# Optimization experiments

Measured on AMD Instinct MI355X. Metric: run time of the kernel, lower is better.

The kernel has to match this reference:

```python
import jax, jax.numpy as jnp
import numpy as np

T, D, I, E, G, LG, K = 2048, 1024, 512, 32, 8, 4, 6
SI = 2 * I  # shared expert inter dim = n_shared_experts * inter_dim
ROUTE_SCALE = 1.0


def setup_inputs() -> dict:
    key = jax.random.key(0)
    ks = jax.random.split(key, 16)
    s = 0.02
    f = jnp.float32
    return {
        "x": jax.random.normal(ks[0], (T, D), f),
        "router_w": jax.random.normal(ks[1], (E, D), f) * s,
        "router_b": jax.random.normal(ks[2], (E,), f) * s,
        "W1": jax.random.normal(ks[3], (E, D, I), f) * s,
        "b1": jax.random.normal(ks[4], (E, I), f) * s,
        "W2": jax.random.normal(ks[5], (E, D, I), f) * s,
        "b2": jax.random.normal(ks[6], (E, I), f) * s,
        "W3": jax.random.normal(ks[7], (E, I, D), f) * s,
        "b3": jax.random.normal(ks[8], (E, D), f) * s,
        "sw1": jax.random.normal(ks[9], (D, SI), f) * s,
        "sb1": jax.random.normal(ks[10], (SI,), f) * s,
        "sw2": jax.random.normal(ks[11], (D, SI), f) * s,
        "sb2": jax.random.normal(ks[12], (SI,), f) * s,
        "sw3": jax.random.normal(ks[13], (SI, D), f) * s,
        "sb3": jax.random.normal(ks[14], (D,), f) * s,
    }


def _route(x, router_w, router_b):
    # Router: softmax scores (fp32), group-limited top-k.
    logits = x @ router_w.T + router_b                      # [T, E]
    scores = jax.nn.softmax(logits.astype(jnp.float32), axis=-1)
    original = scores
    sg = scores.reshape(x.shape[0], G, E // G)              # [T, G, E/G]
    # no router bias -> group score = sum of top-2 expert scores per group
    group_scores = jnp.sum(jax.lax.top_k(sg, 2)[0], axis=-1)  # [T, G]
    _, gidx = jax.lax.top_k(group_scores, LG)               # [T, LG]
    keep = jnp.zeros((x.shape[0], G), bool).at[jnp.arange(x.shape[0])[:, None], gidx].set(True)
    masked = jnp.where(keep[:, :, None], sg, -jnp.inf).reshape(x.shape[0], E)
    _, idx = jax.lax.top_k(masked, K)                       # [T, K]
    vals = jnp.take_along_axis(original, idx, axis=1) * ROUTE_SCALE
    return vals.astype(x.dtype), idx


def reference(x, router_w, router_b, W1, b1, W2, b2, W3, b3, sw1, sb1, sw2, sb2, sw3, sb3):
    vals, idx = _route(x, router_w, router_b)
    # dense gate matrix [T, E]; top-k indices per row are distinct
    gates = jnp.zeros((x.shape[0], E), x.dtype).at[jnp.arange(x.shape[0])[:, None], idx].set(vals)
    # routed experts: Expert(x) = W3 @ silu(w1(x) * w2(x))
    h1 = jnp.einsum('td,edi->tei', x, W1) + b1              # [T, E, I]
    h2 = jnp.einsum('td,edi->tei', x, W2) + b2
    h = jax.nn.silu(h1 * h2)
    y = jnp.einsum('tei,eid->td', h * gates[:, :, None], W3) + gates @ b3
    # shared expert
    z = jax.nn.silu((x @ sw1 + sb1) * (x @ sw2 + sb2)) @ sw3 + sb3
    return y + z
```

## Files before the change

kernel.cpp:

```cpp
#include <hip/hip_runtime.h>
#include <hip/hip_bf16.h>
#include <math.h>

#define T_CONST 2048
#define D_CONST 1024
#define I_CONST 512
#define SI_CONST 1024
#define E_CONST 32
#define G_CONST 8
#define LG_CONST 4
#define KSEL 6

#define BM 128
#define BN 64
#define BK 32

typedef __attribute__((ext_vector_type(8))) short short8;
typedef __attribute__((ext_vector_type(4))) float floatx4;

__device__ inline unsigned pack_bf16(float a, float b) {
  __hip_bfloat162 h = __float22bfloat162_rn(float2{a, b});
  return *reinterpret_cast<unsigned*>(&h);
}

__global__ __launch_bounds__(256) void router_kernel(
    const float* __restrict__ x, const float* __restrict__ rw,
    const float* __restrict__ rb, int* __restrict__ counts,
    int* __restrict__ slots, float* __restrict__ gatel) {
  int t = blockIdx.x;
  __shared__ float sx[D_CONST];
  __shared__ float slog[E_CONST];
  int tid = threadIdx.x;
  for (int i = tid; i < D_CONST; i += 256) sx[i] = x[(size_t)t * D_CONST + i];
  __syncthreads();
  int e = tid >> 3, l8 = tid & 7;
  float s = 0.f;
  const float* rwp = rw + (size_t)e * D_CONST;
  for (int d = l8; d < D_CONST; d += 8) s += sx[d] * rwp[d];
  s += __shfl_xor(s, 4, 8);
  s += __shfl_xor(s, 2, 8);
  s += __shfl_xor(s, 1, 8);
  if (l8 == 0) slog[e] = s + rb[e];
  __syncthreads();
  if (tid == 0) {
    float sc[E_CONST];
    float mx = -1e30f;
    for (int i = 0; i < E_CONST; ++i) mx = fmaxf(mx, slog[i]);
    float sum = 0.f;
    for (int i = 0; i < E_CONST; ++i) { sc[i] = expf(slog[i] - mx); sum += sc[i]; }
    float inv = 1.f / sum;
    for (int i = 0; i < E_CONST; ++i) sc[i] *= inv;
    float gs[G_CONST];
    for (int g = 0; g < G_CONST; ++g) {
      float m1 = -1e30f, m2 = -1e30f;
      for (int j = 0; j < 4; ++j) {
        float v = sc[g * 4 + j];
        if (v > m1) { m2 = m1; m1 = v; }
        else if (v > m2) { m2 = v; }
      }
      gs[g] = m1 + m2;
    }
    bool keep[G_CONST];
    for (int g = 0; g < G_CONST; ++g) keep[g] = false;
    for (int r = 0; r < LG_CONST; ++r) {
      int bi = -1; float bv = -1e30f;
      for (int g = 0; g < G_CONST; ++g)
        if (!keep[g] && gs[g] > bv) { bv = gs[g]; bi = g; }
      keep[bi] = true;
    }
    bool taken[E_CONST];
    for (int i = 0; i < E_CONST; ++i) taken[i] = false;
    for (int r = 0; r < KSEL; ++r) {
      int bi = -1; float bv = -1e30f;
      for (int i = 0; i < E_CONST; ++i)
        if (keep[i >> 2] && !taken[i] && sc[i] > bv) { bv = sc[i]; bi = i; }
      taken[bi] = true;
      int pos = atomicAdd(&counts[bi], 1);
      slots[bi * T_CONST + pos] = t * KSEL + r;
      gatel[bi * T_CONST + pos] = sc[bi];
    }
  }
}

template <bool GATHER>
__global__ __launch_bounds__(256, 2) void up_proj_mfma(
    const float* __restrict__ X, const float* __restrict__ W1g,
    const float* __restrict__ W2g, const float* __restrict__ bias1,
    const float* __restrict__ bias2, const int* __restrict__ counts,
    const int* __restrict__ slots, __hip_bfloat16* __restrict__ Hout, int N) {
  const int e = GATHER ? blockIdx.z : 0;
  const int cnt = GATHER ? counts[e] : T_CONST;
  const int m0 = blockIdx.y * BM;
  if (m0 >= cnt) return;
  const int n0 = blockIdx.x * BN;

  __shared__ short As[4 * BM * 8];
  __shared__ short Bs1[4 * BN * 8];
  __shared__ short Bs2[4 * BN * 8];
  __shared__ int srow[BM];
  __shared__ int sdst[BM];

  const int tid = threadIdx.x;
  for (int i = tid; i < BM; i += 256) {
    int r = m0 + i;
    bool valid = r < cnt;
    if (GATHER) {
      int sl = valid ? slots[e * T_CONST + r] : 0;
      srow[i] = valid ? sl / KSEL : 0;
      sdst[i] = valid ? sl : -1;
    } else {
      srow[i] = valid ? r : 0;
      sdst[i] = valid ? r : -1;
    }
  }
  __syncthreads();

  const float* Wp1 = W1g + (size_t)e * D_CONST * N;
  const float* Wp2 = W2g + (size_t)e * D_CONST * N;

  const int lane = tid & 63;
  const int wave = tid >> 6;
  const int wm = wave & 1, wn = wave >> 1;
  const int l15 = lane & 15, quad = lane >> 4;

  floatx4 acc1[4][2] = {};
  floatx4 acc2[4][2] = {};

  const int akq = tid & 7;
  const float* aptr[4];
#pragma unroll
  for (int it = 0; it < 4; ++it) {
    int m = (tid >> 3) + 32 * it;
    aptr[it] = X + (size_t)srow[m] * D_CONST + akq * 4;
  }
  const int bkp = tid >> 4, bnq = tid & 15;
  const int bc = bkp >> 2, bj = (bkp & 3) * 2;

  for (int kk = 0; kk < D_CONST; kk += BK) {
#pragma unroll
    for (int it = 0; it < 4; ++it) {
      int m = (tid >> 3) + 32 * it;
      float4 f = *(const float4*)(aptr[it] + kk);
      uint2 u;
      u.x = pack_bf16(f.x, f.y);
      u.y = pack_bf16(f.z, f.w);
      int c = akq >> 1, h = akq & 1;
      *(uint2*)&As[(c * BM + m) * 8 + h * 4] = u;
    }
    {
      int k = kk + bkp * 2;
      int n = n0 + bnq * 4;
      const float* p1 = Wp1 + (size_t)k * N + n;
      const float* p2 = Wp2 + (size_t)k * N + n;
      float4 r0 = *(const float4*)p1;
      float4 r1 = *(const float4*)(p1 + N);
      float4 q0 = *(const float4*)p2;
      float4 q1 = *(const float4*)(p2 + N);
      int nb = bnq * 4;
      *(unsigned*)&Bs1[(bc * BN + nb + 0) * 8 + bj] = pack_bf16(r0.x, r1.x);
      *(unsigned*)&Bs1[(bc * BN + nb + 1) * 8 + bj] = pack_bf16(r0.y, r1.y);
      *(unsigned*)&Bs1[(bc * BN + nb + 2) * 8 + bj] = pack_bf16(r0.z, r1.z);
      *(unsigned*)&Bs1[(bc * BN + nb + 3) * 8 + bj] = pack_bf16(r0.w, r1.w);
      *(unsigned*)&Bs2[(bc * BN + nb + 0) * 8 + bj] = pack_bf16(q0.x, q1.x);
      *(unsigned*)&Bs2[(bc * BN + nb + 1) * 8 + bj] = pack_bf16(q0.y, q1.y);
      *(unsigned*)&Bs2[(bc * BN + nb + 2) * 8 + bj] = pack_bf16(q0.z, q1.z);
      *(unsigned*)&Bs2[(bc * BN + nb + 3) * 8 + bj] = pack_bf16(q0.w, q1.w);
    }
    __syncthreads();

    short8 a[4];
#pragma unroll
    for (int mi = 0; mi < 4; ++mi)
      a[mi] = *(const short8*)&As[(quad * BM + wm * 64 + mi * 16 + l15) * 8];
#pragma unroll
    for (int ni = 0; ni < 2; ++ni) {
      short8 b1 = *(const short8*)&Bs1[(quad * BN + wn * 32 + ni * 16 + l15) * 8];
      short8 b2 = *(const short8*)&Bs2[(quad * BN + wn * 32 + ni * 16 + l15) * 8];
#pragma unroll
      for (int mi = 0; mi < 4; ++mi) {
        acc1[mi][ni] = __builtin_amdgcn_mfma_f32_16x16x32_bf16(a[mi], b1, acc1[mi][ni], 0, 0, 0);
        acc2[mi][ni] = __builtin_amdgcn_mfma_f32_16x16x32_bf16(a[mi], b2, acc2[mi][ni], 0, 0, 0);
      }
    }
    __syncthreads();
  }

  const float* bb1 = bias1 + (size_t)e * N + n0;
  const float* bb2 = bias2 + (size_t)e * N + n0;
#pragma unroll
  for (int mi = 0; mi < 4; ++mi) {
#pragma unroll
    for (int ni = 0; ni < 2; ++ni) {
      int n = wn * 32 + ni * 16 + l15;
      float c1 = bb1[n], c2 = bb2[n];
#pragma unroll
      for (int reg = 0; reg < 4; ++reg) {
        int row = wm * 64 + mi * 16 + quad * 4 + reg;
        int dst = sdst[row];
        if (dst < 0) continue;
        float h1 = acc1[mi][ni][reg] + c1;
        float h2 = acc2[mi][ni][reg] + c2;
        float p = h1 * h2;
        float s = p / (1.f + expf(-p));
        Hout[(size_t)dst * N + n0 + n] = __float2bfloat16(s);
      }
    }
  }
}

template <bool ROUTED>
__global__ __launch_bounds__(256, 2) void down_proj_mfma(
    const __hip_bfloat16* __restrict__ Hin, const float* __restrict__ Wd,
    const float* __restrict__ bd, const int* __restrict__ counts,
    const int* __restrict__ slots, const float* __restrict__ gatel,
    float* __restrict__ Out, int Kdim) {
  const int e = ROUTED ? blockIdx.z : 0;
  const int cnt = ROUTED ? counts[e] : T_CONST;
  const int m0 = blockIdx.y * BM;
  if (m0 >= cnt) return;
  const int n0 = blockIdx.x * BN;

  __shared__ short As[4 * BM * 8];
  __shared__ short Bs[4 * BN * 8];
  __shared__ int ssrc[BM];
  __shared__ int stok[BM];
  __shared__ float sg[BM];

  const int tid = threadIdx.x;
  for (int i = tid; i < BM; i += 256) {
    int r = m0 + i;
    bool valid = r < cnt;
    if (ROUTED) {
      int sl = valid ? slots[e * T_CONST + r] : 0;
      ssrc[i] = sl;
      stok[i] = valid ? (sl / KSEL) : -1;
      sg[i] = valid ? gatel[e * T_CONST + r] : 0.f;
    } else {
      ssrc[i] = valid ? r : 0;
      stok[i] = valid ? r : -1;
      sg[i] = 1.f;
    }
  }
  __syncthreads();

  const float* Wp = Wd + (size_t)e * Kdim * D_CONST;

  const int lane = tid & 63;
  const int wave = tid >> 6;
  const int wm = wave & 1, wn = wave >> 1;
  const int l15 = lane & 15, quad = lane >> 4;

  floatx4 acc[4][2] = {};

  const int ako = tid & 3;
  const __hip_bfloat16* aptr[2];
#pragma unroll
  for (int it = 0; it < 2; ++it) {
    int m = (tid >> 2) + 64 * it;
    aptr[it] = Hin + (size_t)ssrc[m] * Kdim + ako * 8;
  }
  const int bkp = tid >> 4, bnq = tid & 15;
  const int bc = bkp >> 2, bj = (bkp & 3) * 2;

  for (int kk = 0; kk < Kdim; kk += BK) {
#pragma unroll
    for (int it = 0; it < 2; ++it) {
      int m = (tid >> 2) + 64 * it;
      uint4 v = *(const uint4*)(aptr[it] + kk);
      *(uint4*)&As[(ako * BM + m) * 8] = v;
    }
    {
      int k = kk + bkp * 2;
      int n = n0 + bnq * 4;
      const float* p = Wp + (size_t)k * D_CONST + n;
      float4 r0 = *(const float4*)p;
      float4 r1 = *(const float4*)(p + D_CONST);
      int nb = bnq * 4;
      *(unsigned*)&Bs[(bc * BN + nb + 0) * 8 + bj] = pack_bf16(r0.x, r1.x);
      *(unsigned*)&Bs[(bc * BN + nb + 1) * 8 + bj] = pack_bf16(r0.y, r1.y);
      *(unsigned*)&Bs[(bc * BN + nb + 2) * 8 + bj] = pack_bf16(r0.z, r1.z);
      *(unsigned*)&Bs[(bc * BN + nb + 3) * 8 + bj] = pack_bf16(r0.w, r1.w);
    }
    __syncthreads();

    short8 a[4];
#pragma unroll
    for (int mi = 0; mi < 4; ++mi)
      a[mi] = *(const short8*)&As[(quad * BM + wm * 64 + mi * 16 + l15) * 8];
#pragma unroll
    for (int ni = 0; ni < 2; ++ni) {
      short8 b = *(const short8*)&Bs[(quad * BN + wn * 32 + ni * 16 + l15) * 8];
#pragma unroll
      for (int mi = 0; mi < 4; ++mi)
        acc[mi][ni] = __builtin_amdgcn_mfma_f32_16x16x32_bf16(a[mi], b, acc[mi][ni], 0, 0, 0);
    }
    __syncthreads();
  }

#pragma unroll
  for (int mi = 0; mi < 4; ++mi) {
#pragma unroll
    for (int ni = 0; ni < 2; ++ni) {
      int n = n0 + wn * 32 + ni * 16 + l15;
      float bias = ROUTED ? bd[(size_t)e * D_CONST + n] : bd[n];
#pragma unroll
      for (int reg = 0; reg < 4; ++reg) {
        int row = wm * 64 + mi * 16 + quad * 4 + reg;
        int tok = stok[row];
        if (tok < 0) continue;
        if (ROUTED) {
          float v = sg[row] * (acc[mi][ni][reg] + bias);
          atomicAdd(&Out[(size_t)tok * D_CONST + n], v);
        } else {
          Out[(size_t)tok * D_CONST + n] = acc[mi][ni][reg] + bias;
        }
      }
    }
  }
}

extern "C" void kernel_launch(void* const* d_in, const int* in_sizes, int n_in,
                              void* d_out, int out_size, void* d_ws, size_t ws_size,
                              hipStream_t stream) {
  const float* x   = (const float*)d_in[0];
  const float* rw  = (const float*)d_in[1];
  const float* rb  = (const float*)d_in[2];
  const float* W1  = (const float*)d_in[3];
  const float* b1  = (const float*)d_in[4];
  const float* W2  = (const float*)d_in[5];
  const float* b2  = (const float*)d_in[6];
  const float* W3  = (const float*)d_in[7];
  const float* b3  = (const float*)d_in[8];
  const float* sw1 = (const float*)d_in[9];
  const float* sb1 = (const float*)d_in[10];
  const float* sw2 = (const float*)d_in[11];
  const float* sb2 = (const float*)d_in[12];
  const float* sw3 = (const float*)d_in[13];
  const float* sb3 = (const float*)d_in[14];
  float* out = (float*)d_out;

  char* w = (char*)d_ws;
  int* counts = (int*)w;
  int* slots = (int*)(w + 256);
  float* gatel = (float*)(w + 256 + E_CONST * T_CONST * 4);
  __hip_bfloat16* Hbuf = (__hip_bfloat16*)(w + 256 + 2 * E_CONST * T_CONST * 4);
  __hip_bfloat16* Hs = (__hip_bfloat16*)(w + 256 + 2 * E_CONST * T_CONST * 4 +
                                         (size_t)T_CONST * KSEL * I_CONST * 2);

  hipMemsetAsync(counts, 0, E_CONST * sizeof(int), stream);
  router_kernel<<<T_CONST, 256, 0, stream>>>(x, rw, rb, counts, slots, gatel);
  up_proj_mfma<true><<<dim3(I_CONST / BN, T_CONST / BM, E_CONST), 256, 0, stream>>>(
      x, W1, W2, b1, b2, counts, slots, Hbuf, I_CONST);
  up_proj_mfma<false><<<dim3(SI_CONST / BN, T_CONST / BM, 1), 256, 0, stream>>>(
      x, sw1, sw2, sb1, sb2, nullptr, nullptr, Hs, SI_CONST);
  down_proj_mfma<false><<<dim3(D_CONST / BN, T_CONST / BM, 1), 256, 0, stream>>>(
      Hs, sw3, sb3, nullptr, nullptr, nullptr, out, SI_CONST);
  down_proj_mfma<true><<<dim3(D_CONST / BN, T_CONST / BM, E_CONST), 256, 0, stream>>>(
      Hbuf, W3, b3, counts, slots, gatel, out, I_CONST);
}
```

Before: 545.4 us.

## Pre-transpose weights to bf16, use direct global-to-LDS loads, parallelize router

```diff
diff --git a/kernel.cpp b/kernel.cpp
--- a/kernel.cpp
+++ b/kernel.cpp
@@ -13,7 +13,7 @@
 
 #define BM 128
 #define BN 64
-#define BK 32
+#define BK 64
 
 typedef __attribute__((ext_vector_type(8))) short short8;
 typedef __attribute__((ext_vector_type(4))) float floatx4;
@@ -23,165 +23,238 @@
   return *reinterpret_cast<unsigned*>(&h);
 }
 
-__global__ __launch_bounds__(256) void router_kernel(
-    const float* __restrict__ x, const float* __restrict__ rw,
+__device__ inline void gload16(const void* g, void* l) {
+  __builtin_amdgcn_global_load_lds(
+      (const __attribute__((address_space(1))) unsigned int*)g,
+      (__attribute__((address_space(3))) unsigned int*)l, 16, 0, 0);
+}
+
+__global__ __launch_bounds__(256) void cvt_x(const float* __restrict__ in,
+                                             __hip_bfloat16* __restrict__ out) {
+  size_t i = ((size_t)blockIdx.x * 256 + threadIdx.x) * 4;
+  float4 v = *(const float4*)&in[i];
+  uint2 u{pack_bf16(v.x, v.y), pack_bf16(v.z, v.w)};
+  *(uint2*)&out[i] = u;
+}
+
+__global__ __launch_bounds__(256) void cvt_rwt(const float* __restrict__ rw,
+                                               float* __restrict__ rwt) {
+  int i = blockIdx.x * 256 + threadIdx.x;
+  int d = i >> 5, e = i & 31;
+  rwt[d * 32 + e] = rw[e * D_CONST + d];
+}
+
+__global__ __launch_bounds__(256) void transpose_all(
+    const float* __restrict__ W1, const float* __restrict__ W2,
+    const float* __restrict__ W3, const float* __restrict__ sw1,
+    const float* __restrict__ sw2, const float* __restrict__ sw3,
+    __hip_bfloat16* __restrict__ W1t, __hip_bfloat16* __restrict__ W2t,
+    __hip_bfloat16* __restrict__ W3t, __hip_bfloat16* __restrict__ sw1t,
+    __hip_bfloat16* __restrict__ sw2t, __hip_bfloat16* __restrict__ sw3t) {
+  __shared__ float tile[64][65];
+  int b = blockIdx.x;
+  const float* in;
+  __hip_bfloat16* out;
+  int K, N, k0, n0;
+  if (b < 8192) {
+    int local = b & 4095;
+    int mat = local >> 7, rem = local & 127;
+    K = 1024; N = 512;
+    in = ((b < 4096) ? W1 : W2) + (size_t)mat * (1024 * 512);
+    out = ((b < 4096) ? W1t : W2t) + (size_t)mat * (1024 * 512);
+    n0 = (rem & 7) * 64; k0 = (rem >> 3) * 64;
+  } else if (b < 12288) {
+    int local = b - 8192;
+    int mat = local >> 7, rem = local & 127;
+    K = 512; N = 1024;
+    in = W3 + (size_t)mat * (512 * 1024);
+    out = W3t + (size_t)mat * (512 * 1024);
+    n0 = (rem & 15) * 64; k0 = (rem >> 4) * 64;
+  } else {
+    int local = b - 12288;
+    int which = local >> 8, rem = local & 255;
+    K = 1024; N = 1024;
+    in = which == 0 ? sw1 : which == 1 ? sw2 : sw3;
+    out = which == 0 ? sw1t : which == 1 ? sw2t : sw3t;
+    n0 = (rem & 15) * 64; k0 = (rem >> 4) * 64;
+  }
+  int tid = threadIdx.x;
+  int tr = tid >> 4, tc4 = (tid & 15) * 4;
+#pragma unroll
+  for (int i = 0; i < 4; ++i) {
+    float4 v = *(const float4*)&in[(size_t)(k0 + tr + 16 * i) * N + n0 + tc4];
+    tile[tr + 16 * i][tc4 + 0] = v.x;
+    tile[tr + 16 * i][tc4 + 1] = v.y;
+    tile[tr + 16 * i][tc4 + 2] = v.z;
+    tile[tr + 16 * i][tc4 + 3] = v.w;
+  }
+  __syncthreads();
+#pragma unroll
+  for (int i = 0; i < 4; ++i) {
+    int n = tr + 16 * i;
+    unsigned lo = pack_bf16(tile[tc4 + 0][n], tile[tc4 + 1][n]);
+    unsigned hi = pack_bf16(tile[tc4 + 2][n], tile[tc4 + 3][n]);
+    uint2 u{lo, hi};
+    *(uint2*)&out[(size_t)(n0 + n) * K + k0 + tc4] = u;
+  }
+}
+
+__global__ __launch_bounds__(256) void router2(
+    const float* __restrict__ x, const float* __restrict__ rwt,
     const float* __restrict__ rb, int* __restrict__ counts,
     int* __restrict__ slots, float* __restrict__ gatel) {
-  int t = blockIdx.x;
-  __shared__ float sx[D_CONST];
-  __shared__ float slog[E_CONST];
-  int tid = threadIdx.x;
-  for (int i = tid; i < D_CONST; i += 256) sx[i] = x[(size_t)t * D_CONST + i];
-  __syncthreads();
-  int e = tid >> 3, l8 = tid & 7;
+  const int lane = threadIdx.x & 63;
+  const int wv = threadIdx.x >> 6;
+  const int t = blockIdx.x * 4 + wv;
+  const int e = lane & 31, h = lane >> 5;
+  const float* xp = x + (size_t)t * D_CONST;
   float s = 0.f;
-  const float* rwp = rw + (size_t)e * D_CONST;
-  for (int d = l8; d < D_CONST; d += 8) s += sx[d] * rwp[d];
-  s += __shfl_xor(s, 4, 8);
-  s += __shfl_xor(s, 2, 8);
-  s += __shfl_xor(s, 1, 8);
-  if (l8 == 0) slog[e] = s + rb[e];
-  __syncthreads();
-  if (tid == 0) {
-    float sc[E_CONST];
-    float mx = -1e30f;
-    for (int i = 0; i < E_CONST; ++i) mx = fmaxf(mx, slog[i]);
-    float sum = 0.f;
-    for (int i = 0; i < E_CONST; ++i) { sc[i] = expf(slog[i] - mx); sum += sc[i]; }
-    float inv = 1.f / sum;
-    for (int i = 0; i < E_CONST; ++i) sc[i] *= inv;
-    float gs[G_CONST];
-    for (int g = 0; g < G_CONST; ++g) {
-      float m1 = -1e30f, m2 = -1e30f;
-      for (int j = 0; j < 4; ++j) {
-        float v = sc[g * 4 + j];
-        if (v > m1) { m2 = m1; m1 = v; }
-        else if (v > m2) { m2 = v; }
-      }
-      gs[g] = m1 + m2;
-    }
-    bool keep[G_CONST];
-    for (int g = 0; g < G_CONST; ++g) keep[g] = false;
-    for (int r = 0; r < LG_CONST; ++r) {
-      int bi = -1; float bv = -1e30f;
-      for (int g = 0; g < G_CONST; ++g)
-        if (!keep[g] && gs[g] > bv) { bv = gs[g]; bi = g; }
-      keep[bi] = true;
-    }
-    bool taken[E_CONST];
-    for (int i = 0; i < E_CONST; ++i) taken[i] = false;
-    for (int r = 0; r < KSEL; ++r) {
-      int bi = -1; float bv = -1e30f;
-      for (int i = 0; i < E_CONST; ++i)
-        if (keep[i >> 2] && !taken[i] && sc[i] > bv) { bv = sc[i]; bi = i; }
-      taken[bi] = true;
-      int pos = atomicAdd(&counts[bi], 1);
-      slots[bi * T_CONST + pos] = t * KSEL + r;
-      gatel[bi * T_CONST + pos] = sc[bi];
-    }
+#pragma unroll 8
+  for (int d = h; d < D_CONST; d += 2) s = fmaf(xp[d], rwt[d * 32 + e], s);
+  s += __shfl_xor(s, 32);
+  s += rb[e];
+  float mx = s;
+#pragma unroll
+  for (int m = 16; m >= 1; m >>= 1) mx = fmaxf(mx, __shfl_xor(mx, m));
+  float p = expf(s - mx);
+  float sum = p;
+#pragma unroll
+  for (int m = 16; m >= 1; m >>= 1) sum += __shfl_xor(sum, m);
+  float sc = p / sum;
+  float a = sc, bb = __shfl_xor(a, 1);
+  float hi = fmaxf(a, bb), lo = fminf(a, bb);
+  float oh = __shfl_xor(hi, 2), ol = __shfl_xor(lo, 2);
+  float gs = fmaxf(fmaxf(hi + oh, hi + lo), oh + ol);
+  const int g = e >> 2;
+  unsigned keep = 0;
+  float gv = gs;
+#pragma unroll
+  for (int r = 0; r < LG_CONST; ++r) {
+    float v = gv;
+    int gi = g;
+#pragma unroll
+    for (int m = 16; m >= 1; m >>= 1) {
+      float ov = __shfl_xor(v, m);
+      int og = __shfl_xor(gi, m);
+      if (ov > v || (ov == v && og < gi)) { v = ov; gi = og; }
+    }
+    keep |= 1u << gi;
+    if (g == gi) gv = -1e30f;
+  }
+  float cand = ((keep >> g) & 1u) ? sc : -1e30f;
+  int sel_e = -1;
+  float sel_v = 0.f;
+#pragma unroll
+  for (int r = 0; r < KSEL; ++r) {
+    float v = cand;
+    int ei = e;
+#pragma unroll
+    for (int m = 16; m >= 1; m >>= 1) {
+      float ov = __shfl_xor(v, m);
+      int oe = __shfl_xor(ei, m);
+      if (ov > v || (ov == v && oe < ei)) { v = ov; ei = oe; }
+    }
+    if (lane == r) { sel_e = ei; sel_v = v; }
+    if (e == ei) cand = -1e30f;
+  }
+  if (lane < KSEL) {
+    int pos = atomicAdd(&counts[sel_e], 1);
+    slots[sel_e * T_CONST + pos] = t * KSEL + lane;
+    gatel[sel_e * T_CONST + pos] = sel_v;
   }
 }
 
 template <bool GATHER>
-__global__ __launch_bounds__(256, 2) void up_proj_mfma(
-    const float* __restrict__ X, const float* __restrict__ W1g,
-    const float* __restrict__ W2g, const float* __restrict__ bias1,
+__global__ __launch_bounds__(256, 2) void up_mfma2(
+    const __hip_bfloat16* __restrict__ Abf, const __hip_bfloat16* __restrict__ B1t,
+    const __hip_bfloat16* __restrict__ B2t, const float* __restrict__ bias1,
     const float* __restrict__ bias2, const int* __restrict__ counts,
-    const int* __restrict__ slots, __hip_bfloat16* __restrict__ Hout, int N) {
+    const int* __restrict__ slots, __hip_bfloat16* __restrict__ Hout,
+    int N, int Kd) {
   const int e = GATHER ? blockIdx.z : 0;
   const int cnt = GATHER ? counts[e] : T_CONST;
   const int m0 = blockIdx.y * BM;
   if (m0 >= cnt) return;
   const int n0 = blockIdx.x * BN;
 
-  __shared__ short As[4 * BM * 8];
-  __shared__ short Bs1[4 * BN * 8];
-  __shared__ short Bs2[4 * BN * 8];
+  __shared__ short As[8 * BM * 8];
+  __shared__ short Bs1[8 * BN * 8];
+  __shared__ short Bs2[8 * BN * 8];
   __shared__ int srow[BM];
   __shared__ int sdst[BM];
 
   const int tid = threadIdx.x;
-  for (int i = tid; i < BM; i += 256) {
-    int r = m0 + i;
+  const int lane = tid & 63, wv = tid >> 6;
+  if (tid < BM) {
+    int r = m0 + tid;
     bool valid = r < cnt;
     if (GATHER) {
       int sl = valid ? slots[e * T_CONST + r] : 0;
-      srow[i] = valid ? sl / KSEL : 0;
-      sdst[i] = valid ? sl : -1;
+      srow[tid] = valid ? sl / KSEL : 0;
+      sdst[tid] = valid ? sl : -1;
     } else {
-      srow[i] = valid ? r : 0;
-      sdst[i] = valid ? r : -1;
+      srow[tid] = valid ? r : 0;
+      sdst[tid] = valid ? r : -1;
     }
   }
   __syncthreads();
 
-  const float* Wp1 = W1g + (size_t)e * D_CONST * N;
-  const float* Wp2 = W2g + (size_t)e * D_CONST * N;
-
-  const int lane = tid & 63;
-  const int wave = tid >> 6;
-  const int wm = wave & 1, wn = wave >> 1;
+  const char* agp[4];
+  short* alds[4];
+  const char* bgp[4];
+  short* blds[4];
+  {
+    int row0 = srow[lane], row1 = srow[64 + lane];
+#pragma unroll
+    for (int i = 0; i < 4; ++i) {
+      int kc = 2 * wv + (i >> 1);
+      int mh = i & 1;
+      agp[i] = (const char*)(Abf + (size_t)(mh ? row1 : row0) * Kd + kc * 8);
+      alds[i] = (short*)As + (kc * BM + mh * 64 + lane) * 8;
+    }
+    const __hip_bfloat16* Bsel = (wv < 2 ? B1t : B2t) + (size_t)e * N * Kd;
+    short* Lsel = (wv < 2) ? (short*)Bs1 : (short*)Bs2;
+    int wl = wv & 1;
+#pragma unroll
+    for (int i = 0; i < 4; ++i) {
+      int kc = wl * 4 + i;
+      bgp[i] = (const char*)(Bsel + (size_t)(n0 + lane) * Kd + kc * 8);
+      blds[i] = Lsel + (kc * BN + lane) * 8;
+    }
+  }
+
   const int l15 = lane & 15, quad = lane >> 4;
-
+  const int wm = wv & 1, wn = wv >> 1;
   floatx4 acc1[4][2] = {};
   floatx4 acc2[4][2] = {};
-
-  const int akq = tid & 7;
-  const float* aptr[4];
-#pragma unroll
-  for (int it = 0; it < 4; ++it) {
-    int m = (tid >> 3) + 32 * it;
-    aptr[it] = X + (size_t)srow[m] * D_CONST + akq * 4;
-  }
-  const int bkp = tid >> 4, bnq = tid & 15;
-  const int bc = bkp >> 2, bj = (bkp & 3) * 2;
-
-  for (int kk = 0; kk < D_CONST; kk += BK) {
-#pragma unroll
-    for (int it = 0; it < 4; ++it) {
-      int m = (tid >> 3) + 32 * it;
-      float4 f = *(const float4*)(aptr[it] + kk);
-      uint2 u;
-      u.x = pack_bf16(f.x, f.y);
-      u.y = pack_bf16(f.z, f.w);
-      int c = akq >> 1, h = akq & 1;
-      *(uint2*)&As[(c * BM + m) * 8 + h * 4] = u;
-    }
-    {
-      int k = kk + bkp * 2;
-      int n = n0 + bnq * 4;
-      const float* p1 = Wp1 + (size_t)k * N + n;
-      const float* p2 = Wp2 + (size_t)k * N + n;
-      float4 r0 = *(const float4*)p1;
-      float4 r1 = *(const float4*)(p1 + N);
-      float4 q0 = *(const float4*)p2;
-      float4 q1 = *(const float4*)(p2 + N);
-      int nb = bnq * 4;
-      *(unsigned*)&Bs1[(bc * BN + nb + 0) * 8 + bj] = pack_bf16(r0.x, r1.x);
-      *(unsigned*)&Bs1[(bc * BN + nb + 1) * 8 + bj] = pack_bf16(r0.y, r1.y);
-      *(unsigned*)&Bs1[(bc * BN + nb + 2) * 8 + bj] = pack_bf16(r0.z, r1.z);
-      *(unsigned*)&Bs1[(bc * BN + nb + 3) * 8 + bj] = pack_bf16(r0.w, r1.w);
-      *(unsigned*)&Bs2[(bc * BN + nb + 0) * 8 + bj] = pack_bf16(q0.x, q1.x);
-      *(unsigned*)&Bs2[(bc * BN + nb + 1) * 8 + bj] = pack_bf16(q0.y, q1.y);
-      *(unsigned*)&Bs2[(bc * BN + nb + 2) * 8 + bj] = pack_bf16(q0.z, q1.z);
-      *(unsigned*)&Bs2[(bc * BN + nb + 3) * 8 + bj] = pack_bf16(q0.w, q1.w);
-    }
+  const int kiter = Kd / BK;
+
+  for (int it = 0; it < kiter; ++it) {
+#pragma unroll
+    for (int i = 0; i < 4; ++i) gload16(agp[i], alds[i]);
+#pragma unroll
+    for (int i = 0; i < 4; ++i) gload16(bgp[i], blds[i]);
+#pragma unroll
+    for (int i = 0; i < 4; ++i) { agp[i] += BK * 2; bgp[i] += BK * 2; }
     __syncthreads();
-
-    short8 a[4];
-#pragma unroll
-    for (int mi = 0; mi < 4; ++mi)
-      a[mi] = *(const short8*)&As[(quad * BM + wm * 64 + mi * 16 + l15) * 8];
-#pragma unroll
-    for (int ni = 0; ni < 2; ++ni) {
-      short8 b1 = *(const short8*)&Bs1[(quad * BN + wn * 32 + ni * 16 + l15) * 8];
-      short8 b2 = *(const short8*)&Bs2[(quad * BN + wn * 32 + ni * 16 + l15) * 8];
-#pragma unroll
-      for (int mi = 0; mi < 4; ++mi) {
-        acc1[mi][ni] = __builtin_amdgcn_mfma_f32_16x16x32_bf16(a[mi], b1, acc1[mi][ni], 0, 0, 0);
-        acc2[mi][ni] = __builtin_amdgcn_mfma_f32_16x16x32_bf16(a[mi], b2, acc2[mi][ni], 0, 0, 0);
+    short8 a[2][4];
+#pragma unroll
+    for (int s = 0; s < 2; ++s)
+#pragma unroll
+      for (int mi = 0; mi < 4; ++mi)
+        a[s][mi] = *(const short8*)&As[((s * 4 + quad) * BM + wm * 64 + mi * 16 + l15) * 8];
+#pragma unroll
+    for (int s = 0; s < 2; ++s)
+#pragma unroll
+      for (int ni = 0; ni < 2; ++ni) {
+        short8 b1 = *(const short8*)&Bs1[((s * 4 + quad) * BN + wn * 32 + ni * 16 + l15) * 8];
+        short8 b2 = *(const short8*)&Bs2[((s * 4 + quad) * BN + wn * 32 + ni * 16 + l15) * 8];
+#pragma unroll
+        for (int mi = 0; mi < 4; ++mi) {
+          acc1[mi][ni] = __builtin_amdgcn_mfma_f32_16x16x32_bf16(a[s][mi], b1, acc1[mi][ni], 0, 0, 0);
+          acc2[mi][ni] = __builtin_amdgcn_mfma_f32_16x16x32_bf16(a[s][mi], b2, acc2[mi][ni], 0, 0, 0);
+        }
       }
-    }
     __syncthreads();
   }
 
@@ -201,99 +274,101 @@
         float h1 = acc1[mi][ni][reg] + c1;
         float h2 = acc2[mi][ni][reg] + c2;
         float p = h1 * h2;
-        float s = p / (1.f + expf(-p));
-        Hout[(size_t)dst * N + n0 + n] = __float2bfloat16(s);
+        float sv = p / (1.f + expf(-p));
+        Hout[(size_t)dst * N + n0 + n] = __float2bfloat16(sv);
       }
     }
   }
 }
 
 template <bool ROUTED>
-__global__ __launch_bounds__(256, 2) void down_proj_mfma(
-    const __hip_bfloat16* __restrict__ Hin, const float* __restrict__ Wd,
+__global__ __launch_bounds__(256, 2) void down_mfma2(
+    const __hip_bfloat16* __restrict__ Hin, const __hip_bfloat16* __restrict__ Bt,
     const float* __restrict__ bd, const int* __restrict__ counts,
     const int* __restrict__ slots, const float* __restrict__ gatel,
-    float* __restrict__ Out, int Kdim) {
+    float* __restrict__ Out, int Kd) {
   const int e = ROUTED ? blockIdx.z : 0;
   const int cnt = ROUTED ? counts[e] : T_CONST;
   const int m0 = blockIdx.y * BM;
   if (m0 >= cnt) return;
   const int n0 = blockIdx.x * BN;
 
-  __shared__ short As[4 * BM * 8];
-  __shared__ short Bs[4 * BN * 8];
+  __shared__ short As[8 * BM * 8];
+  __shared__ short Bs[8 * BN * 8];
   __shared__ int ssrc[BM];
   __shared__ int stok[BM];
   __shared__ float sg[BM];
 
   const int tid = threadIdx.x;
-  for (int i = tid; i < BM; i += 256) {
-    int r = m0 + i;
+  const int lane = tid & 63, wv = tid >> 6;
+  if (tid < BM) {
+    int r = m0 + tid;
     bool valid = r < cnt;
     if (ROUTED) {
       int sl = valid ? slots[e * T_CONST + r] : 0;
-      ssrc[i] = sl;
-      stok[i] = valid ? (sl / KSEL) : -1;
-      sg[i] = valid ? gatel[e * T_CONST + r] : 0.f;
+      ssrc[tid] = sl;
+      stok[tid] = valid ? (sl / KSEL) : -1;
+      sg[tid] = valid ? gatel[e * T_CONST + r] : 0.f;
     } else {
-      ssrc[i] = valid ? r : 0;
-      stok[i] = valid ? r : -1;
-      sg[i] = 1.f;
+      ssrc[tid] = valid ? r : 0;
+      stok[tid] = valid ? r : -1;
+      sg[tid] = 1.f;
     }
   }
   __syncthreads();
 
-  const float* Wp = Wd + (size_t)e * Kdim * D_CONST;
-
-  const int lane = tid & 63;
-  const int wave = tid >> 6;
-  const int wm = wave & 1, wn = wave >> 1;
+  const char* agp[4];
+  short* alds[4];
+  const char* bgp[2];
+  short* blds[2];
+  {
+    int row0 = ssrc[lane], row1 = ssrc[64 + lane];
+#pragma unroll
+    for (int i = 0; i < 4; ++i) {
+      int kc = 2 * wv + (i >> 1);
+      int mh = i & 1;
+      agp[i] = (const char*)(Hin + (size_t)(mh ? row1 : row0) * Kd + kc * 8);
+      alds[i] = (short*)As + (kc * BM + mh * 64 + lane) * 8;
+    }
+    const __hip_bfloat16* Bsel = Bt + (size_t)e * D_CONST * Kd;
+#pragma unroll
+    for (int i = 0; i < 2; ++i) {
+      int kc = 2 * wv + i;
+      bgp[i] = (const char*)(Bsel + (size_t)(n0 + lane) * Kd + kc * 8);
+      blds[i] = (short*)Bs + (kc * BN + lane) * 8;
+    }
+  }
+
   const int l15 = lane & 15, quad = lane >> 4;
-
+  const int wm = wv & 1, wn = wv >> 1;
   floatx4 acc[4][2] = {};
-
-  const int ako = tid & 3;
-  const __hip_bfloat16* aptr[2];
-#pragma unroll
-  for (int it = 0; it < 2; ++it) {
-    int m = (tid >> 2) + 64 * it;
-    aptr[it] = Hin + (size_t)ssrc[m] * Kdim + ako * 8;
-  }
-  const int bkp = tid >> 4, bnq = tid & 15;
-  const int bc = bkp >> 2, bj = (bkp & 3) * 2;
-
-  for (int kk = 0; kk < Kdim; kk += BK) {
-#pragma unroll
-    for (int it = 0; it < 2; ++it) {
-      int m = (tid >> 2) + 64 * it;
-      uint4 v = *(const uint4*)(aptr[it] + kk);
-      *(uint4*)&As[(ako * BM + m) * 8] = v;
-    }
-    {
-      int k = kk + bkp * 2;
-      int n = n0 + bnq * 4;
-      const float* p = Wp + (size_t)k * D_CONST + n;
-      float4 r0 = *(const float4*)p;
-      float4 r1 = *(const float4*)(p + D_CONST);
-      int nb = bnq * 4;
-      *(unsigned*)&Bs[(bc * BN + nb + 0) * 8 + bj] = pack_bf16(r0.x, r1.x);
-      *(unsigned*)&Bs[(bc * BN + nb + 1) * 8 + bj] = pack_bf16(r0.y, r1.y);
-      *(unsigned*)&Bs[(bc * BN + nb + 2) * 8 + bj] = pack_bf16(r0.z, r1.z);
-      *(unsigned*)&Bs[(bc * BN + nb + 3) * 8 + bj] = pack_bf16(r0.w, r1.w);
-    }
+  const int kiter = Kd / BK;
+
+  for (int it = 0; it < kiter; ++it) {
+#pragma unroll
+    for (int i = 0; i < 4; ++i) gload16(agp[i], alds[i]);
+#pragma unroll
+    for (int i = 0; i < 2; ++i) gload16(bgp[i], blds[i]);
+#pragma unroll
+    for (int i = 0; i < 4; ++i) agp[i] += BK * 2;
+#pragma unroll
+    for (int i = 0; i < 2; ++i) bgp[i] += BK * 2;
     __syncthreads();
-
-    short8 a[4];
-#pragma unroll
-    for (int mi = 0; mi < 4; ++mi)
-      a[mi] = *(const short8*)&As[(quad * BM + wm * 64 + mi * 16 + l15) * 8];
-#pragma unroll
-    for (int ni = 0; ni < 2; ++ni) {
-      short8 b = *(const short8*)&Bs[(quad * BN + wn * 32 + ni * 16 + l15) * 8];
+    short8 a[2][4];
+#pragma unroll
+    for (int s = 0; s < 2; ++s)
 #pragma unroll
       for (int mi = 0; mi < 4; ++mi)
-        acc[mi][ni] = __builtin_amdgcn_mfma_f32_16x16x32_bf16(a[mi], b, acc[mi][ni], 0, 0, 0);
-    }
+        a[s][mi] = *(const short8*)&As[((s * 4 + quad) * BM + wm * 64 + mi * 16 + l15) * 8];
+#pragma unroll
+    for (int s = 0; s < 2; ++s)
+#pragma unroll
+      for (int ni = 0; ni < 2; ++ni) {
+        short8 b = *(const short8*)&Bs[((s * 4 + quad) * BN + wn * 32 + ni * 16 + l15) * 8];
+#pragma unroll
+        for (int mi = 0; mi < 4; ++mi)
+          acc[mi][ni] = __builtin_amdgcn_mfma_f32_16x16x32_bf16(a[s][mi], b, acc[mi][ni], 0, 0, 0);
+      }
     __syncthreads();
   }
 
@@ -340,21 +415,38 @@
   float* out = (float*)d_out;
 
   char* w = (char*)d_ws;
-  int* counts = (int*)w;
-  int* slots = (int*)(w + 256);
-  float* gatel = (float*)(w + 256 + E_CONST * T_CONST * 4);
-  __hip_bfloat16* Hbuf = (__hip_bfloat16*)(w + 256 + 2 * E_CONST * T_CONST * 4);
-  __hip_bfloat16* Hs = (__hip_bfloat16*)(w + 256 + 2 * E_CONST * T_CONST * 4 +
-                                         (size_t)T_CONST * KSEL * I_CONST * 2);
+  size_t off = 0;
+  auto alloc = [&](size_t bytes) {
+    char* p = w + off;
+    off += (bytes + 255) & ~(size_t)255;
+    return p;
+  };
+  int* counts = (int*)alloc(E_CONST * 4);
+  int* slots = (int*)alloc((size_t)E_CONST * T_CONST * 4);
+  float* gatel = (float*)alloc((size_t)E_CONST * T_CONST * 4);
+  float* rwt = (float*)alloc((size_t)D_CONST * E_CONST * 4);
+  __hip_bfloat16* x_bf = (__hip_bfloat16*)alloc((size_t)T_CONST * D_CONST * 2);
+  __hip_bfloat16* W1t = (__hip_bfloat16*)alloc((size_t)E_CONST * D_CONST * I_CONST * 2);
+  __hip_bfloat16* W2t = (__hip_bfloat16*)alloc((size_t)E_CONST * D_CONST * I_CONST * 2);
+  __hip_bfloat16* W3t = (__hip_bfloat16*)alloc((size_t)E_CONST * I_CONST * D_CONST * 2);
+  __hip_bfloat16* sw1t = (__hip_bfloat16*)alloc((size_t)D_CONST * SI_CONST * 2);
+  __hip_bfloat16* sw2t = (__hip_bfloat16*)alloc((size_t)D_CONST * SI_CONST * 2);
+  __hip_bfloat16* sw3t = (__hip_bfloat16*)alloc((size_t)SI_CONST * D_CONST * 2);
+  __hip_bfloat16* Hbuf = (__hip_bfloat16*)alloc((size_t)T_CONST * KSEL * I_CONST * 2);
+  __hip_bfloat16* Hs = (__hip_bfloat16*)alloc((size_t)T_CONST * SI_CONST * 2);
 
   hipMemsetAsync(counts, 0, E_CONST * sizeof(int), stream);
-  router_kernel<<<T_CONST, 256, 0, stream>>>(x, rw, rb, counts, slots, gatel);
-  up_proj_mfma<true><<<dim3(I_CONST / BN, T_CONST / BM, E_CONST), 256, 0, stream>>>(
-      x, W1, W2, b1, b2, counts, slots, Hbuf, I_CONST);
-  up_proj_mfma<false><<<dim3(SI_CONST / BN, T_CONST / BM, 1), 256, 0, stream>>>(
-      x, sw1, sw2, sb1, sb2, nullptr, nullptr, Hs, SI_CONST);
-  down_proj_mfma<false><<<dim3(D_CONST / BN, T_CONST / BM, 1), 256, 0, stream>>>(
-      Hs, sw3, sb3, nullptr, nullptr, nullptr, out, SI_CONST);
-  down_proj_mfma<true><<<dim3(D_CONST / BN, T_CONST / BM, E_CONST), 256, 0, stream>>>(
-      Hbuf, W3, b3, counts, slots, gatel, out, I_CONST);
-}
+  cvt_rwt<<<(D_CONST * E_CONST) / 256, 256, 0, stream>>>(rw, rwt);
+  cvt_x<<<(T_CONST * D_CONST) / 1024, 256, 0, stream>>>(x, x_bf);
+  transpose_all<<<13056, 256, 0, stream>>>(W1, W2, W3, sw1, sw2, sw3,
+                                           W1t, W2t, W3t, sw1t, sw2t, sw3t);
+  router2<<<T_CONST / 4, 256, 0, stream>>>(x, rwt, rb, counts, slots, gatel);
+  up_mfma2<true><<<dim3(I_CONST / BN, T_CONST / BM, E_CONST), 256, 0, stream>>>(
+      x_bf, W1t, W2t, b1, b2, counts, slots, Hbuf, I_CONST, D_CONST);
+  up_mfma2<false><<<dim3(SI_CONST / BN, T_CONST / BM, 1), 256, 0, stream>>>(
+      x_bf, sw1t, sw2t, sb1, sb2, nullptr, nullptr, Hs, SI_CONST, D_CONST);
+  down_mfma2<false><<<dim3(D_CONST / BN, T_CONST / BM, 1), 256, 0, stream>>>(
+      Hs, sw3t, sb3, nullptr, nullptr, nullptr, out, SI_CONST);
+  down_mfma2<true><<<dim3(D_CONST / BN, T_CONST / BM, E_CONST), 256, 0, stream>>>(
+      Hbuf, W3t, b3, counts, slots, gatel, out, I_CONST);
+}
```

Result: no change. 537.7 us (-1.4%).
